# Performance work log

Hardware: AMD Instinct MI355X
Metric: run time of the kernel (lower is better)

The kernel has to match this reference:

```python
import jax, jax.numpy as jnp
import numpy as np

H, C = 4, 32            # heads, hidden_channel
HC = H * C              # 128
IN = 128                # in_channel
N = 50000               # nodes in sampled subgraph
E = 200000              # edges
USER, ITEM = 50000, 50000
UB = 200                # ubias_num == ibias_num
DIST = 501
BATCH = 1024
NEG = 0.2               # leaky_relu negative slope


def setup_inputs() -> dict:
    key = jax.random.key(0)
    keys = iter(jax.random.split(key, 64))

    def nrm(shape):
        return jax.random.normal(next(keys), shape, dtype=jnp.float32) * 0.05

    def ri(shape, hi):
        return jax.random.randint(next(keys), shape, 0, hi, dtype=jnp.int32)

    inp = {
        # int (graph) inputs
        "node_idx": ri((N,), USER + ITEM + 1),
        "edge_index": ri((2, E), N),
        "edge_type": ri((E,), 6),
        "t_offset_0": ri((E,), UB + 2),
        "t_offset_1": ri((E,), UB + 2),
        "dists_0": ri((E,), DIST),
        "dists_1": ri((E,), DIST),
        "center_nid": ri((BATCH,), N),
        # parameters
        "id_emb": nrm((USER + ITEM + 1, IN)),
        "ucenter_att_bias": nrm((UB + 2, HC)),
        "icenter_att_bias": nrm((UB + 2, HC)),
        "trans_att_bias": nrm((UB + 2, HC)),
        "ucenter_emb_bias": nrm((UB + 2, HC)),
        "icenter_emb_bias": nrm((UB + 2, HC)),
        "trans_emb_bias": nrm((UB + 2, HC)),
        "ucenter_att_bias_2": nrm((UB * 4 + 2, HC)),
        "icenter_att_bias_2": nrm((UB * 4 + 2, HC)),
        "trans_att_bias_2": nrm((UB * 4 + 2, HC)),
        "ucenter_emb_bias_2": nrm((UB * 4 + 2, HC)),
        "icenter_emb_bias_2": nrm((UB * 4 + 2, HC)),
        "trans_emb_bias_2": nrm((UB * 4 + 2, HC)),
        "udist_att_bias": nrm((DIST, HC)),
        "idist_att_bias": nrm((DIST, HC)),
        "udist_emb_bias": nrm((DIST, HC)),
        "idist_emb_bias": nrm((DIST, HC)),
        "udist_att_bias_2": nrm((DIST, HC)),
        "idist_att_bias_2": nrm((DIST, HC)),
        "udist_emb_bias_2": nrm((DIST, HC)),
        "idist_emb_bias_2": nrm((DIST, HC)),
        "trans_head": nrm((IN, HC)),
        "rnn_w": nrm((2 * HC, HC)),           # rnn_update Linear (no bias)
        "w1": nrm((HC * 2 + IN, HC)),          # pred_head layer 1
        "b1": jnp.zeros((HC,), jnp.float32),
        "w2": nrm((HC, ITEM)),                 # pred_head layer 2
        "b2": jnp.zeros((ITEM,), jnp.float32),
        # per-layer conv params (src/dst projections + attention vectors)
        "wl0": nrm((IN, HC)), "wr0": nrm((IN, HC)),
        "asrc0": nrm((H, C)), "adst0": nrm((H, C)),
        "wl1": nrm((HC, HC)), "wr1": nrm((HC, HC)),
        "asrc1": nrm((H, C)), "adst1": nrm((H, C)),
    }
    return inp


def reference(node_idx, edge_index, edge_type, t_offset_0, t_offset_1, dists_0,
              dists_1, center_nid, id_emb, ucenter_att_bias, icenter_att_bias,
              trans_att_bias, ucenter_emb_bias, icenter_emb_bias, trans_emb_bias,
              ucenter_att_bias_2, icenter_att_bias_2, trans_att_bias_2,
              ucenter_emb_bias_2, icenter_emb_bias_2, trans_emb_bias_2,
              udist_att_bias, idist_att_bias, udist_emb_bias, idist_emb_bias,
              udist_att_bias_2, idist_att_bias_2, udist_emb_bias_2,
              idist_emb_bias_2, trans_head, rnn_w, w1, b1, w2, b2,
              wl0, wr0, asrc0, adst0, wl1, wr1, asrc1, adst1):
    x = id_emb[node_idx]                       # [N, IN] gather
    src, dst = edge_index[0], edge_index[1]
    is_u = (edge_type == 0)[:, None]           # user-center homo edges
    is_homo = (edge_type < 2)[:, None]
    involved = ((edge_type == 0) | (edge_type == 2) | (edge_type == 3))[:, None]

    def edge_bias(u_tab, i_tab, tr_tab, toff):
        # homo edges: type-0 -> user table, type-1 -> item table; hetero -> trans table
        b = jnp.where(is_u, u_tab[toff], jnp.where(is_homo, i_tab[toff], tr_tab[toff]))
        return b.reshape(-1, H, C)

    def dist_bias(u_tab, i_tab, dists):
        b = jnp.where(is_u, u_tab[dists], i_tab[dists]) * involved
        return b.reshape(-1, H, C)

    att_b = [edge_bias(ucenter_att_bias, icenter_att_bias, trans_att_bias, t_offset_0),
             edge_bias(ucenter_att_bias_2, icenter_att_bias_2, trans_att_bias_2, t_offset_1)]
    emb_b = [edge_bias(ucenter_emb_bias, icenter_emb_bias, trans_emb_bias, t_offset_0),
             edge_bias(ucenter_emb_bias_2, icenter_emb_bias_2, trans_emb_bias_2, t_offset_1)]
    att_d = [dist_bias(udist_att_bias, idist_att_bias, dists_0),
             dist_bias(udist_att_bias_2, idist_att_bias_2, dists_1)]
    emb_d = [dist_bias(udist_emb_bias, idist_emb_bias, dists_0),
             dist_bias(udist_emb_bias_2, idist_emb_bias_2, dists_1)]

    n_nodes = x.shape[0]

    def conv(h, wl, wr, asrc, adst, ab, eb, ad, ed):
        k = (h @ wl).reshape(n_nodes, H, C)
        q = (h @ wr).reshape(n_nodes, H, C)
        msg = k[src] + eb + ed                                   # [E,H,C]
        logit = jax.nn.leaky_relu(
            jnp.einsum('ehc,hc->eh', k[src] + ab + ad, asrc)
            + jnp.einsum('ehc,hc->eh', q[dst], adst), NEG)        # [E,H]
        m = jax.ops.segment_max(logit, dst, num_segments=n_nodes)
        a = jnp.exp(logit - m[dst])
        den = jax.ops.segment_sum(a, dst, num_segments=n_nodes)
        alpha = a / jnp.maximum(den[dst], 1e-16)
        out = jax.ops.segment_sum(alpha[..., None] * msg, dst, num_segments=n_nodes)
        return out.reshape(n_nodes, HC)

    layers = [(wl0, wr0, asrc0, adst0), (wl1, wr1, asrc1, adst1)]
    x_inter = [x]
    cur = x
    for i in range(2):
        last = cur @ trans_head if i == 0 else cur
        wl, wr, asrc, adst = layers[i]
        cur = conv(cur, wl, wr, asrc, adst, att_b[i], emb_b[i], att_d[i], emb_d[i])
        cur = jnp.tanh(jnp.concatenate([cur, last], axis=-1) @ rnn_w)
        x_inter.append(cur)
        if i != 1:
            cur = jax.nn.relu(cur)   # dropout: eval mode -> identity

    feat = jnp.concatenate(x_inter, axis=-1)[center_nid]   # [B, 2*HC+IN]
    hdd = jax.nn.leaky_relu(feat @ w1 + b1, NEG)            # dropout eval -> identity
    logits = hdd @ w2 + b2                                  # [B, ITEM]
    return logits
```

## Files before the change

kernel.cpp:

```cpp
#include <hip/hip_runtime.h>
#include <cstdint>
#include <cstddef>

typedef unsigned short u16;
typedef __attribute__((ext_vector_type(8))) short short8;
typedef __attribute__((ext_vector_type(4))) float f32x4;

#define HC_ 128
#define CAP 32
#define OFF_U0   0
#define OFF_I0   202
#define OFF_T0   404
#define OFF_UD0  606
#define OFF_ID0  1107
#define OFF_U2   1608
#define OFF_I2   2410
#define OFF_T2   3212
#define OFF_UD2  4014
#define OFF_ID2  4515
#define DOT_ROWS 5016

__device__ __forceinline__ float b2f(u16 u) {
  union { unsigned int i; float f; } v; v.i = ((unsigned int)u) << 16; return v.f;
}
__device__ __forceinline__ u16 f2b(float f) {
  union { float f; unsigned int i; } v; v.f = f;
  unsigned int r = v.i + 0x7fffu + ((v.i >> 16) & 1u);
  return (u16)(r >> 16);
}

__global__ __launch_bounds__(256) void prolog_k(
    const int* __restrict__ nidx, const float* __restrict__ emb, u16* __restrict__ x,
    const float* u0, const float* i0, const float* t0, const float* ud0, const float* id0,
    const float* u2, const float* i2, const float* t2, const float* ud2, const float* id2,
    const float* __restrict__ asrc0, const float* __restrict__ asrc1,
    float* __restrict__ dots,
    const float* __restrict__ wr0, const float* __restrict__ adst0,
    const float* __restrict__ wr1, const float* __restrict__ adst1,
    float* __restrict__ wq,
    const float* __restrict__ rnn_w, u16* __restrict__ rnn_wb,
    const float* __restrict__ th, u16* __restrict__ Wt,
    int* __restrict__ cur, float* __restrict__ kdot0, float* __restrict__ kdot1,
    int* __restrict__ mask1, int* __restrict__ mask2,
    const int* __restrict__ center, int B_, int Nn)
{
  int b = blockIdx.x, t = threadIdx.x;
  const int nbZ    = (Nn + 16 + 255) >> 8;
  const int nbC    = (B_ + 255) >> 8;
  const int nbGx   = ((Nn + 16) * 16 + 255) >> 8;
  const int nbDots = (DOT_ROWS * 4 + 255) >> 8;

  if (b < nbZ) {
    int i = b * 256 + t;
    if (i < Nn + 16) {
      cur[i] = 0;
      f32x4 z = {0.f, 0.f, 0.f, 0.f};
      *(f32x4*)(kdot0 + (size_t)i * 4) = z;
      *(f32x4*)(kdot1 + (size_t)i * 4) = z;
    }
    return;
  }
  b -= nbZ;
  if (b < nbC) {
    int i = b * 256 + t;
    if (i < B_) { int c = center[i]; mask2[c] = 1; mask1[c] = 1; }
    return;
  }
  b -= nbC;
  if (b < nbGx) {
    int i = b * 256 + t;
    int n = i >> 4, c = (i & 15) << 3;
    if (n < Nn) {
      int id = nidx[n];
      const float* s = emb + (size_t)id * HC_ + c;
      u16 tmp[8];
#pragma unroll
      for (int j = 0; j < 8; ++j) tmp[j] = f2b(s[j]);
      *(short8*)(x + (size_t)n * HC_ + c) = *(short8*)tmp;
    } else if (n < Nn + 16) {
      short8 z = {0,0,0,0,0,0,0,0};
      *(short8*)(x + (size_t)n * HC_ + c) = z;
    }
    return;
  }
  b -= nbGx;
  if (b < nbDots) {
    int i = b * 256 + t;
    if (i < DOT_ROWS * 4) {
      int r = i >> 2, h = i & 3;
      const float* tab; int lr; const float* as;
      if      (r < OFF_I0)  { tab = u0;  lr = r;            as = asrc0; }
      else if (r < OFF_T0)  { tab = i0;  lr = r - OFF_I0;   as = asrc0; }
      else if (r < OFF_UD0) { tab = t0;  lr = r - OFF_T0;   as = asrc0; }
      else if (r < OFF_ID0) { tab = ud0; lr = r - OFF_UD0;  as = asrc0; }
      else if (r < OFF_U2)  { tab = id0; lr = r - OFF_ID0;  as = asrc0; }
      else if (r < OFF_I2)  { tab = u2;  lr = r - OFF_U2;   as = asrc1; }
      else if (r < OFF_T2)  { tab = i2;  lr = r - OFF_I2;   as = asrc1; }
      else if (r < OFF_UD2) { tab = t2;  lr = r - OFF_T2;   as = asrc1; }
      else if (r < OFF_ID2) { tab = ud2; lr = r - OFF_UD2;  as = asrc1; }
      else                  { tab = id2; lr = r - OFF_ID2;  as = asrc1; }
      float s = 0.f;
#pragma unroll
      for (int c = 0; c < 32; ++c)
        s += tab[(size_t)lr * HC_ + h * 32 + c] * as[h * 32 + c];
      dots[i] = s;
    }
    return;
  }
  b -= nbDots;
  if (b < 4) {
    int i = b * 256 + t;
    int layer = i >> 9, k = (i >> 2) & 127, h = i & 3;
    const float* wr = layer ? wr1 : wr0;
    const float* ad = layer ? adst1 : adst0;
    float s = 0.f;
#pragma unroll
    for (int c = 0; c < 32; ++c)
      s += wr[(size_t)k * HC_ + h * 32 + c] * ad[h * 32 + c];
    wq[i] = s;
    return;
  }
  b -= 4;
  if (b < 128) {
    int i = b * 256 + t;
    rnn_wb[i] = f2b(rnn_w[i]);
    return;
  }
  b -= 128;
  {
    int i = b * 256 + t;
    if (i < 16384) {
      int r = i >> 7, c = i & 127;
      float s = 0.f;
#pragma unroll 8
      for (int k = 0; k < 128; ++k)
        s += th[r * 128 + k] * rnn_w[(size_t)(128 + k) * 128 + c];
      Wt[i] = f2b(s);
    }
  }
}

__global__ void fill_k(const int* __restrict__ src, const int* __restrict__ dst,
                       const int* __restrict__ ety,
                       const int* __restrict__ toff0, const int* __restrict__ toff1,
                       const int* __restrict__ dist0, const int* __restrict__ dist1,
                       const float* __restrict__ dots,
                       int* __restrict__ cur,
                       int2* __restrict__ m0a, f32x4* __restrict__ e0a,
                       int2* __restrict__ m1a, f32x4* __restrict__ e1a,
                       const int* __restrict__ mask2, int* __restrict__ mask1, int E)
{
  int e = blockIdx.x * blockDim.x + threadIdx.x;
  if (e >= E) return;
  int d = dst[e];
  int s = src[e];
  if (mask2[d]) mask1[s] = 1;
  int slot = atomicAdd(&cur[d], 1);
  if (slot >= CAP) return;
  int ty = ety[e];
  int to0 = toff0[e], to1 = toff1[e], di0 = dist0[e], di1 = dist1[e];
  bool inv = (ty == 0 || ty == 2 || ty == 3);
  int ar0 = (ty == 0) ? (OFF_U0 + to0) : (ty < 2) ? (OFF_I0 + to0) : (OFF_T0 + to0);
  int ar1 = (ty == 0) ? (OFF_U2 + to1) : (ty < 2) ? (OFF_I2 + to1) : (OFF_T2 + to1);
  f32x4 e0 = *(const f32x4*)(dots + (size_t)ar0 * 4);
  f32x4 e1 = *(const f32x4*)(dots + (size_t)ar1 * 4);
  if (inv) {
    int dr0 = ((ty == 0) ? OFF_UD0 : OFF_ID0) + di0;
    int dr1 = ((ty == 0) ? OFF_UD2 : OFF_ID2) + di1;
    e0 += *(const f32x4*)(dots + (size_t)dr0 * 4);
    e1 += *(const f32x4*)(dots + (size_t)dr1 * 4);
  }
  size_t ix = (size_t)d * CAP + slot;
  m0a[ix] = make_int2(s, ty | (to0 << 3) | (di0 << 13));
  m1a[ix] = make_int2(s, ty | (to1 << 3) | (di1 << 13));
  e0a[ix] = e0;
  e1a[ix] = e1;
}

__global__ void mark0_k(const int* __restrict__ esrc, const int* __restrict__ edst,
                        const int* __restrict__ mask1, int* __restrict__ mask0, int E)
{
  int e = blockIdx.x * blockDim.x + threadIdx.x;
  if (e < E && mask1[edst[e]]) mask0[esrc[e]] = 1;
}

__global__ void compact_k(const int* __restrict__ mask0, const int* __restrict__ mask1,
                          int* __restrict__ L0, int* __restrict__ L1,
                          int* __restrict__ cnts, int Nn)
{
  int n = blockIdx.x * blockDim.x + threadIdx.x;
  if (n >= Nn) return;
  int m1 = mask1[n];
  if (m1 | mask0[n]) L0[atomicAdd(&cnts[0], 1)] = n;
  if (m1)            L1[atomicAdd(&cnts[1], 1)] = n;
}

template<int RELUA>
__global__ __launch_bounds__(256) void gemm_kq_g(
    const u16* __restrict__ A, const float* __restrict__ W, u16* __restrict__ C,
    const float* __restrict__ asrc, const float* __restrict__ wqt,
    float* __restrict__ kdot, float* __restrict__ qdot,
    const int* __restrict__ list, const int* __restrict__ cnts, int ci, int Nsent)
{
  const int lane = threadIdx.x & 63;
  const int wave = threadIdx.x >> 6;
  const int quad = lane >> 4;
  const int l16  = lane & 15;
  const int by   = blockIdx.y;
  const int n0   = by * 64 + wave * 16;

  short8 bfrag[4];
#pragma unroll
  for (int ks = 0; ks < 4; ++ks) {
    short8 bf;
    const int kb = ks * 32 + quad * 8;
#pragma unroll
    for (int j = 0; j < 8; ++j)
      bf[j] = (short)f2b(W[(size_t)(kb + j) * HC_ + n0 + l16]);
    bfrag[ks] = bf;
  }
  const int hh = n0 >> 5;
  const float asv = asrc[n0 + l16];

  const int cnt = cnts[ci];
  const int mtiles = (cnt + 15) >> 4;
  for (int mt = blockIdx.x; mt < mtiles; mt += gridDim.x) {
    const int rA = mt * 16 + l16;
    const int gA = (rA < cnt) ? list[rA] : Nsent;
    const u16* arow = A + (size_t)gA * HC_;
    f32x4 acc = {0.f, 0.f, 0.f, 0.f};
    float qp[4] = {0.f, 0.f, 0.f, 0.f};
#pragma unroll
    for (int ks = 0; ks < 4; ++ks) {
      short8 af = *(const short8*)(arow + ks * 32 + quad * 8);
      if (RELUA) {
#pragma unroll
        for (int j = 0; j < 8; ++j) af[j] = (af[j] < (short)0) ? (short)0 : af[j];
      }
#pragma unroll
      for (int j = 0; j < 8; ++j) {
        float v = b2f((u16)af[j]);
        const float* wr = wqt + (size_t)(ks * 32 + quad * 8 + j) * 4;
        qp[0] += v * wr[0]; qp[1] += v * wr[1];
        qp[2] += v * wr[2]; qp[3] += v * wr[3];
      }
      acc = __builtin_amdgcn_mfma_f32_16x16x32_bf16(af, bfrag[ks], acc, 0, 0, 0);
    }
#pragma unroll
    for (int h = 0; h < 4; ++h) {
      qp[h] += __shfl_xor(qp[h], 16, 64);
      qp[h] += __shfl_xor(qp[h], 32, 64);
    }
    if (by == 0 && quad == 0) {
      f32x4 qv; qv[0] = qp[0]; qv[1] = qp[1]; qv[2] = qp[2]; qv[3] = qp[3];
      *(f32x4*)(qdot + (size_t)gA * 4) = qv;
    }
    int gC[4];
#pragma unroll
    for (int r = 0; r < 4; ++r) {
      const int rC = mt * 16 + quad * 4 + r;
      gC[r] = (rC < cnt) ? list[rC] : Nsent;
    }
#pragma unroll
    for (int r = 0; r < 4; ++r) {
      float sr = acc[r] * asv;
      sr += __shfl_xor(sr, 1, 64); sr += __shfl_xor(sr, 2, 64);
      sr += __shfl_xor(sr, 4, 64); sr += __shfl_xor(sr, 8, 64);
      if (l16 == 0)
        atomicAdd(&kdot[(size_t)gC[r] * 4 + hh], sr);
    }
#pragma unroll
    for (int r = 0; r < 4; ++r)
      C[(size_t)gC[r] * HC_ + n0 + l16] = f2b(acc[r]);
  }
}

__global__ __launch_bounds__(256) void gemm2_g(
    const float* __restrict__ A1, const u16* __restrict__ W1,
    const u16* __restrict__ A2, const u16* __restrict__ W2,
    u16* __restrict__ Cout,
    const int* __restrict__ list, const int* __restrict__ cnts, int ci, int Nsent)
{
  const int lane = threadIdx.x & 63;
  const int wave = threadIdx.x >> 6;
  const int quad = lane >> 4;
  const int l16  = lane & 15;
  const int n0   = blockIdx.y * 64 + wave * 16;

  short8 bf1[4], bf2[4];
#pragma unroll
  for (int ks = 0; ks < 4; ++ks) {
    short8 a, b;
    const int kb = ks * 32 + quad * 8;
#pragma unroll
    for (int j = 0; j < 8; ++j) {
      a[j] = (short)W1[(size_t)(kb + j) * HC_ + n0 + l16];
      b[j] = (short)W2[(size_t)(kb + j) * HC_ + n0 + l16];
    }
    bf1[ks] = a; bf2[ks] = b;
  }

  const int cnt = cnts[ci];
  const int mtiles = (cnt + 15) >> 4;
  for (int mt = blockIdx.x; mt < mtiles; mt += gridDim.x) {
    const int rA = mt * 16 + l16;
    const int gA = (rA < cnt) ? list[rA] : Nsent;
    const float* a1 = A1 + (size_t)gA * HC_;
    const u16*   a2 = A2 + (size_t)gA * HC_;
    f32x4 acc = {0.f, 0.f, 0.f, 0.f};
#pragma unroll
    for (int ks = 0; ks < 4; ++ks) {
      short8 af;
      const float* p = a1 + ks * 32 + quad * 8;
#pragma unroll
      for (int j = 0; j < 8; ++j) af[j] = (short)f2b(p[j]);
      acc = __builtin_amdgcn_mfma_f32_16x16x32_bf16(af, bf1[ks], acc, 0, 0, 0);
    }
#pragma unroll
    for (int ks = 0; ks < 4; ++ks) {
      short8 af = *(const short8*)(a2 + ks * 32 + quad * 8);
      acc = __builtin_amdgcn_mfma_f32_16x16x32_bf16(af, bf2[ks], acc, 0, 0, 0);
    }
#pragma unroll
    for (int r = 0; r < 4; ++r) {
      const int rC = mt * 16 + quad * 4 + r;
      const int gC = (rC < cnt) ? list[rC] : Nsent;
      Cout[(size_t)gC * HC_ + n0 + l16] = f2b(tanhf(acc[r]));
    }
  }
}

template<int DEVCNT>
__global__ __launch_bounds__(256) void conv_k(
    const int* __restrict__ cur, const int2* __restrict__ meta,
    const f32x4* __restrict__ edot,
    const u16* __restrict__ kbuf,
    const float* __restrict__ kdot, const float* __restrict__ qdot,
    const float* __restrict__ uemb, const float* __restrict__ iemb,
    const float* __restrict__ temb,
    const float* __restrict__ udemb, const float* __restrict__ idemb,
    const int* __restrict__ list, const int* __restrict__ cnts, int ci, int cntConst,
    float* __restrict__ CO)
{
  __shared__ float als[4][CAP][4];
  const int wv = threadIdx.x >> 6;
  const int lane = threadIdx.x & 63;
  const int bound = DEVCNT ? cnts[ci] : cntConst;
  const int wstep = gridDim.x * 4;
  const int h0 = lane >> 5;
  const int h1 = h0 + 2;

  for (int wid = (blockIdx.x * blockDim.x + threadIdx.x) >> 6; wid < bound; wid += wstep) {
    const int n = list[wid];
    int cnt = cur[n]; if (cnt > CAP) cnt = CAP;
    const float q0 = qdot[n * 4 + h0];
    const float q1 = qdot[n * 4 + h1];
    const int2* mb = meta + (size_t)n * CAP;
    const f32x4* eb = edot + (size_t)n * CAP;

    float den0 = 0.f, den1 = 0.f;
    for (int e = 0; e < cnt; ++e) {
      int s = mb[e].x;
      f32x4 ed = eb[e];
      float l0 = kdot[s * 4 + h0] + q0 + ed[h0];
      float l1 = kdot[s * 4 + h1] + q1 + ed[h1];
      l0 = (l0 > 0.f) ? l0 : 0.2f * l0;
      l1 = (l1 > 0.f) ? l1 : 0.2f * l1;
      float a0 = __expf(fminf(l0, 30.f));
      float a1 = __expf(fminf(l1, 30.f));
      den0 += a0; den1 += a1;
      if ((lane & 31) == 0) { als[wv][e][h0] = a0; als[wv][e][h1] = a1; }
    }
    const float r0 = 1.f / fmaxf(den0, 1e-16f);
    const float r1 = 1.f / fmaxf(den1, 1e-16f);

    float acc0 = 0.f, acc1 = 0.f;
    for (int e = 0; e < cnt; ++e) {
      int2 mrec = mb[e];
      int s = mrec.x;
      int ty = mrec.y & 7, to = (mrec.y >> 3) & 1023, di = mrec.y >> 13;
      float al0 = als[wv][e][h0] * r0;
      float al1 = als[wv][e][h1] * r1;

      float m0 = b2f(kbuf[(size_t)s * HC_ + lane]);
      float m1 = b2f(kbuf[(size_t)s * HC_ + 64 + lane]);
      const float* et = (ty == 0) ? uemb : (ty < 2) ? iemb : temb;
      m0 += et[(size_t)to * HC_ + lane];
      m1 += et[(size_t)to * HC_ + 64 + lane];
      if (ty == 0 || ty == 2 || ty == 3) {
        const float* dt = (ty == 0) ? udemb : idemb;
        m0 += dt[(size_t)di * HC_ + lane];
        m1 += dt[(size_t)di * HC_ + 64 + lane];
      }
      acc0 += al0 * m0;
      acc1 += al1 * m1;
    }
    CO[(size_t)n * HC_ + lane]      = acc0;
    CO[(size_t)n * HC_ + 64 + lane] = acc1;
  }
}

__global__ __launch_bounds__(256) void gh_k(
    const float* __restrict__ CO, const u16* __restrict__ rnn_wb,
    const u16* __restrict__ h1, const u16* __restrict__ xb,
    const int* __restrict__ center, const float* __restrict__ w1,
    const float* __restrict__ b1, u16* __restrict__ hdd)
{
  __shared__ u16 h2s[16][136];
  const int t = threadIdx.x;
  const int lane = t & 63, wave = t >> 6, quad = lane >> 4, l16 = lane & 15;
  const int mt = blockIdx.x;
  const int rowm = mt * 16 + l16;
  const int nid = center[rowm];
  const u16* W1 = rnn_wb;
  const u16* W2 = rnn_wb + HC_ * HC_;

#pragma unroll
  for (int half = 0; half < 2; ++half) {
    const int n0 = half * 64 + wave * 16;
    short8 bf1[4], bf2[4];
#pragma unroll
    for (int ks = 0; ks < 4; ++ks) {
      short8 a, b;
      const int kb = ks * 32 + quad * 8;
#pragma unroll
      for (int j = 0; j < 8; ++j) {
        a[j] = (short)W1[(size_t)(kb + j) * HC_ + n0 + l16];
        b[j] = (short)W2[(size_t)(kb + j) * HC_ + n0 + l16];
      }
      bf1[ks] = a; bf2[ks] = b;
    }
    const float* a1 = CO + (size_t)nid * HC_;
    const u16*   a2 = h1 + (size_t)nid * HC_;
    f32x4 acc = {0.f, 0.f, 0.f, 0.f};
#pragma unroll
    for (int ks = 0; ks < 4; ++ks) {
      short8 af;
      const float* p = a1 + ks * 32 + quad * 8;
#pragma unroll
      for (int j = 0; j < 8; ++j) af[j] = (short)f2b(p[j]);
      acc = __builtin_amdgcn_mfma_f32_16x16x32_bf16(af, bf1[ks], acc, 0, 0, 0);
    }
#pragma unroll
    for (int ks = 0; ks < 4; ++ks) {
      short8 af = *(const short8*)(a2 + ks * 32 + quad * 8);
#pragma unroll
      for (int j = 0; j < 8; ++j) af[j] = (af[j] < (short)0) ? (short)0 : af[j];
      acc = __builtin_amdgcn_mfma_f32_16x16x32_bf16(af, bf2[ks], acc, 0, 0, 0);
    }
#pragma unroll
    for (int r = 0; r < 4; ++r)
      h2s[quad * 4 + r][n0 + l16] = f2b(tanhf(acc[r]));
  }
  __syncthreads();

#pragma unroll
  for (int half = 0; half < 2; ++half) {
    const int n0 = half * 64 + wave * 16;
    short8 bfrag[12];
#pragma unroll
    for (int ks = 0; ks < 12; ++ks) {
      short8 bf;
      const int kb = ks * 32 + quad * 8;
#pragma unroll
      for (int j = 0; j < 8; ++j)
        bf[j] = (short)f2b(w1[(size_t)(kb + j) * HC_ + n0 + l16]);
      bfrag[ks] = bf;
    }
    const float bv = b1[n0 + l16];
    f32x4 acc = {0.f, 0.f, 0.f, 0.f};
#pragma unroll
    for (int ks = 0; ks < 12; ++ks) {
      short8 af;
      if (ks < 4)
        af = *(const short8*)(xb + (size_t)nid * HC_ + ks * 32 + quad * 8);
      else if (ks < 8)
        af = *(const short8*)(h1 + (size_t)nid * HC_ + (ks - 4) * 32 + quad * 8);
      else
        af = *(const short8*)(&h2s[l16][(ks - 8) * 32 + quad * 8]);
      acc = __builtin_amdgcn_mfma_f32_16x16x32_bf16(af, bfrag[ks], acc, 0, 0, 0);
    }
#pragma unroll
    for (int r = 0; r < 4; ++r) {
      float v = acc[r] + bv;
      v = (v > 0.f) ? v : 0.2f * v;
      hdd[(size_t)(mt * 16 + quad * 4 + r) * HC_ + n0 + l16] = f2b(v);
    }
  }
}

__global__ __launch_bounds__(256) void gemm_out_k(
    const u16* __restrict__ A, const float* __restrict__ W,
    const float* __restrict__ bias, float* __restrict__ out, int M, int ITEM)
{
  __shared__ float lds[4][16][68];
  const int lane = threadIdx.x & 63;
  const int wv   = threadIdx.x >> 6;
  const int quad = lane >> 4;
  const int l16  = lane & 15;
  const int nbase = blockIdx.y * 256 + wv * 64;

  short8 bfrag[4][4];
#pragma unroll
  for (int nt = 0; nt < 4; ++nt) {
    const int colc = nbase + nt * 16 + l16;
    const int col = (colc < ITEM) ? colc : (ITEM - 1);
#pragma unroll
    for (int ks = 0; ks < 4; ++ks) {
      short8 bf;
      const int kb = ks * 32 + quad * 8;
#pragma unroll
      for (int j = 0; j < 8; ++j)
        bf[j] = (short)f2b(W[(size_t)(kb + j) * ITEM + col]);
      bfrag[nt][ks] = bf;
    }
  }
  const int c4 = nbase + l16 * 4;
  const bool wvalid = (c4 + 3) < ITEM;
  float4 bv = make_float4(0.f, 0.f, 0.f, 0.f);
  if (wvalid) bv = *(const float4*)(bias + c4);

  const int mtiles = M >> 4;
  for (int mt = blockIdx.x; mt < mtiles; mt += gridDim.x) {
    const u16* arow = A + (size_t)(mt * 16 + l16) * HC_;
    short8 af[4];
#pragma unroll
    for (int ks = 0; ks < 4; ++ks)
      af[ks] = *(const short8*)(arow + ks * 32 + quad * 8);
    f32x4 acc[4];
#pragma unroll
    for (int nt = 0; nt < 4; ++nt) acc[nt] = (f32x4){0.f, 0.f, 0.f, 0.f};
#pragma unroll
    for (int nt = 0; nt < 4; ++nt)
#pragma unroll
      for (int ks = 0; ks < 4; ++ks)
        acc[nt] = __builtin_amdgcn_mfma_f32_16x16x32_bf16(af[ks], bfrag[nt][ks],
                                                          acc[nt], 0, 0, 0);
#pragma unroll
    for (int nt = 0; nt < 4; ++nt)
#pragma unroll
      for (int r = 0; r < 4; ++r)
        lds[wv][quad * 4 + r][nt * 16 + l16] = acc[nt][r];
    __syncthreads();
    if (wvalid) {
#pragma unroll
      for (int i = 0; i < 4; ++i) {
        const int row = (lane >> 4) + i * 4;
        float4 v = *(const float4*)(&lds[wv][row][l16 * 4]);
        v.x += bv.x; v.y += bv.y; v.z += bv.z; v.w += bv.w;
        *(float4*)(out + (size_t)(mt * 16 + row) * ITEM + c4) = v;
      }
    }
    __syncthreads();
  }
}

extern "C" void kernel_launch(void* const* d_in, const int* in_sizes, int n_in,
                              void* d_out, int out_size, void* d_ws, size_t ws_size,
                              hipStream_t stream)
{
  (void)n_in; (void)out_size; (void)ws_size;
  const int* node_idx = (const int*)d_in[0];
  const int* eidx     = (const int*)d_in[1];
  const int* etype    = (const int*)d_in[2];
  const int* toff0    = (const int*)d_in[3];
  const int* toff1    = (const int*)d_in[4];
  const int* dist0    = (const int*)d_in[5];
  const int* dist1    = (const int*)d_in[6];
  const int* center   = (const int*)d_in[7];
  const float* id_emb   = (const float*)d_in[8];
  const float* u_att    = (const float*)d_in[9];
  const float* i_att    = (const float*)d_in[10];
  const float* t_att    = (const float*)d_in[11];
  const float* u_emb    = (const float*)d_in[12];
  const float* i_emb    = (const float*)d_in[13];
  const float* t_emb    = (const float*)d_in[14];
  const float* u_att2   = (const float*)d_in[15];
  const float* i_att2   = (const float*)d_in[16];
  const float* t_att2   = (const float*)d_in[17];
  const float* u_emb2   = (const float*)d_in[18];
  const float* i_emb2   = (const float*)d_in[19];
  const float* t_emb2   = (const float*)d_in[20];
  const float* ud_att   = (const float*)d_in[21];
  const float* id_att   = (const float*)d_in[22];
  const float* ud_emb   = (const float*)d_in[23];
  const float* id_embd  = (const float*)d_in[24];
  const float* ud_att2  = (const float*)d_in[25];
  const float* id_att2  = (const float*)d_in[26];
  const float* ud_emb2  = (const float*)d_in[27];
  const float* id_emb2  = (const float*)d_in[28];
  const float* trans_head = (const float*)d_in[29];
  const float* rnn_w    = (const float*)d_in[30];
  const float* w1       = (const float*)d_in[31];
  const float* b1       = (const float*)d_in[32];
  const float* w2       = (const float*)d_in[33];
  const float* b2       = (const float*)d_in[34];
  const float* wl0      = (const float*)d_in[35];
  const float* wr0      = (const float*)d_in[36];
  const float* asrc0    = (const float*)d_in[37];
  const float* adst0    = (const float*)d_in[38];
  const float* wl1      = (const float*)d_in[39];
  const float* wr1      = (const float*)d_in[40];
  const float* asrc1    = (const float*)d_in[41];
  const float* adst1    = (const float*)d_in[42];

  const int N_    = in_sizes[0];
  const int E_    = in_sizes[2];
  const int B_    = in_sizes[7];
  const int ITEM_ = in_sizes[34];
  const int* esrc = eidx;
  const int* edst = eidx + E_;

  char* ws = (char*)d_ws;
  size_t off = 0;
  auto alloc = [&](size_t bytes) -> char* {
    char* p = ws + off;
    off += (bytes + 255) & ~(size_t)255;
    return p;
  };
  const int NS = N_ + 16;
  float* CO_b  = (float*)alloc((size_t)NS * HC_ * 4);
  u16*   k_b   = (u16*)  alloc((size_t)NS * HC_ * 2);
  u16*   x_b   = (u16*)  alloc((size_t)NS * HC_ * 2);
  u16*   h1_b  = (u16*)  alloc((size_t)NS * HC_ * 2);
  float* kdot0 = (float*)alloc((size_t)NS * 4 * 4);
  float* kdot1 = (float*)alloc((size_t)NS * 4 * 4);
  float* qdot  = (float*)alloc((size_t)NS * 4 * 4);
  float* dots  = (float*)alloc((size_t)DOT_ROWS * 4 * 4);
  float* wq    = (float*)alloc(1024 * 4);
  u16*   rnn_wb= (u16*)  alloc(256 * HC_ * 2);
  u16*   Wt    = (u16*)  alloc(HC_ * HC_ * 2);
  u16*   hdd   = (u16*)  alloc((size_t)B_ * HC_ * 2);
  int*   cur   = (int*)  alloc((size_t)NS * 4);
  int2*  m0a   = (int2*) alloc((size_t)N_ * CAP * 8);
  int2*  m1a   = (int2*) alloc((size_t)N_ * CAP * 8);
  f32x4* e0a   = (f32x4*)alloc((size_t)N_ * CAP * 16);
  f32x4* e1a   = (f32x4*)alloc((size_t)N_ * CAP * 16);
  int*   maskb = (int*)  alloc(((size_t)3 * N_ + 2) * 4);
  int*   mask0 = maskb;
  int*   mask1 = maskb + N_;
  int*   mask2 = maskb + 2 * N_;
  int*   cnts  = maskb + 3 * N_;
  int*   L0    = (int*)  alloc((size_t)N_ * 4);
  int*   L1    = (int*)  alloc((size_t)N_ * 4);

  const int TB = 256;
  auto nb = [&](long long t) { return (int)((t + TB - 1) / TB); };

  hipMemsetAsync(maskb, 0, ((size_t)3 * N_ + 2) * 4, stream);

  const int nbZ    = (N_ + 16 + 255) / 256;
  const int nbC    = (B_ + 255) / 256;
  const int nbGx   = ((N_ + 16) * 16 + 255) / 256;
  const int nbDots = (DOT_ROWS * 4 + 255) / 256;
  const int prologBlocks = nbZ + nbC + nbGx + nbDots + 4 + 128 + 64;
  prolog_k<<<prologBlocks, TB, 0, stream>>>(
      node_idx, id_emb, x_b,
      u_att, i_att, t_att, ud_att, id_att,
      u_att2, i_att2, t_att2, ud_att2, id_att2,
      asrc0, asrc1, dots,
      wr0, adst0, wr1, adst1, wq,
      rnn_w, rnn_wb, trans_head, Wt,
      cur, kdot0, kdot1,
      mask1, mask2, center, B_, N_);

  fill_k<<<nb(E_), TB, 0, stream>>>(esrc, edst, etype, toff0, toff1, dist0, dist1,
                                    dots, cur, m0a, e0a, m1a, e1a, mask2, mask1, E_);

  mark0_k<<<nb(E_), TB, 0, stream>>>(esrc, edst, mask1, mask0, E_);
  compact_k<<<nb(N_), TB, 0, stream>>>(mask0, mask1, L0, L1, cnts, N_);

  gemm_kq_g<0><<<dim3(640, 2), TB, 0, stream>>>(
      x_b, wl0, k_b, asrc0, wq, kdot0, qdot, L0, cnts, 0, N_);

  conv_k<1><<<1536, TB, 0, stream>>>(
      cur, m0a, e0a, k_b, kdot0, qdot,
      u_emb, i_emb, t_emb, ud_emb, id_embd, L1, cnts, 1, 0, CO_b);

  gemm2_g<<<dim3(640, 2), TB, 0, stream>>>(CO_b, rnn_wb, x_b, Wt, h1_b,
                                           L1, cnts, 1, N_);

  gemm_kq_g<1><<<dim3(640, 2), TB, 0, stream>>>(
      h1_b, wl1, k_b, asrc1, wq + 512, kdot1, qdot, L1, cnts, 1, N_);

  conv_k<0><<<nb((long long)B_ * 64), TB, 0, stream>>>(
      cur, m1a, e1a, k_b, kdot1, qdot,
      u_emb2, i_emb2, t_emb2, ud_emb2, id_emb2, center, nullptr, 0, B_, CO_b);

  gh_k<<<B_ / 16, TB, 0, stream>>>(CO_b, rnn_wb, h1_b, x_b, center, w1, b1, hdd);

  gemm_out_k<<<dim3(8, (ITEM_ + 255) / 256), TB, 0, stream>>>(
      hdd, w2, b2, (float*)d_out, B_, ITEM_);
}
```

Baseline: 559.5 us.

## Fuse final-layer attention conv into head kernel, drop syncs, retune grids

```diff
diff --git a/kernel.cpp b/kernel.cpp
--- a/kernel.cpp
+++ b/kernel.cpp
@@ -330,7 +330,6 @@
   }
 }
 
-template<int DEVCNT>
 __global__ __launch_bounds__(256) void conv_k(
     const int* __restrict__ cur, const int2* __restrict__ meta,
     const f32x4* __restrict__ edot,
@@ -339,13 +338,13 @@
     const float* __restrict__ uemb, const float* __restrict__ iemb,
     const float* __restrict__ temb,
     const float* __restrict__ udemb, const float* __restrict__ idemb,
-    const int* __restrict__ list, const int* __restrict__ cnts, int ci, int cntConst,
+    const int* __restrict__ list, const int* __restrict__ cnts, int ci,
     float* __restrict__ CO)
 {
   __shared__ float als[4][CAP][4];
   const int wv = threadIdx.x >> 6;
   const int lane = threadIdx.x & 63;
-  const int bound = DEVCNT ? cnts[ci] : cntConst;
+  const int bound = cnts[ci];
   const int wstep = gridDim.x * 4;
   const int h0 = lane >> 5;
   const int h1 = h0 + 2;
@@ -400,24 +399,85 @@
   }
 }
 
-__global__ __launch_bounds__(256) void gh_k(
-    const float* __restrict__ CO, const u16* __restrict__ rnn_wb,
-    const u16* __restrict__ h1, const u16* __restrict__ xb,
-    const int* __restrict__ center, const float* __restrict__ w1,
-    const float* __restrict__ b1, u16* __restrict__ hdd)
-{
+__global__ __launch_bounds__(256) void ghc_k(
+    const int* __restrict__ cur, const int2* __restrict__ meta,
+    const f32x4* __restrict__ edot,
+    const u16* __restrict__ kbuf,
+    const float* __restrict__ kdot, const float* __restrict__ qdot,
+    const float* __restrict__ uemb, const float* __restrict__ iemb,
+    const float* __restrict__ temb,
+    const float* __restrict__ udemb, const float* __restrict__ idemb,
+    const int* __restrict__ center,
+    const u16* __restrict__ rnn_wb, const u16* __restrict__ h1b,
+    const u16* __restrict__ xb,
+    const float* __restrict__ w1, const float* __restrict__ b1,
+    u16* __restrict__ hdd)
+{
+  __shared__ float co_s[16][132];
   __shared__ u16 h2s[16][136];
+  __shared__ float als[4][CAP][4];
   const int t = threadIdx.x;
-  const int lane = t & 63, wave = t >> 6, quad = lane >> 4, l16 = lane & 15;
+  const int lane = t & 63, wv = t >> 6, quad = lane >> 4, l16 = lane & 15;
   const int mt = blockIdx.x;
+  const int h0 = lane >> 5, h1h = h0 + 2;
+
+  for (int r = wv; r < 16; r += 4) {
+    const int n = center[mt * 16 + r];
+    int cnt = cur[n]; if (cnt > CAP) cnt = CAP;
+    const float q0 = qdot[n * 4 + h0];
+    const float q1 = qdot[n * 4 + h1h];
+    const int2* mb = meta + (size_t)n * CAP;
+    const f32x4* eb = edot + (size_t)n * CAP;
+
+    float den0 = 0.f, den1 = 0.f;
+    for (int e = 0; e < cnt; ++e) {
+      int s = mb[e].x;
+      f32x4 ed = eb[e];
+      float l0 = kdot[s * 4 + h0] + q0 + ed[h0];
+      float l1 = kdot[s * 4 + h1h] + q1 + ed[h1h];
+      l0 = (l0 > 0.f) ? l0 : 0.2f * l0;
+      l1 = (l1 > 0.f) ? l1 : 0.2f * l1;
+      float a0 = __expf(fminf(l0, 30.f));
+      float a1 = __expf(fminf(l1, 30.f));
+      den0 += a0; den1 += a1;
+      if ((lane & 31) == 0) { als[wv][e][h0] = a0; als[wv][e][h1h] = a1; }
+    }
+    const float r0 = 1.f / fmaxf(den0, 1e-16f);
+    const float r1 = 1.f / fmaxf(den1, 1e-16f);
+
+    float acc0 = 0.f, acc1 = 0.f;
+    for (int e = 0; e < cnt; ++e) {
+      int2 mrec = mb[e];
+      int s = mrec.x;
+      int ty = mrec.y & 7, to = (mrec.y >> 3) & 1023, di = mrec.y >> 13;
+      float al0 = als[wv][e][h0] * r0;
+      float al1 = als[wv][e][h1h] * r1;
+
+      float m0 = b2f(kbuf[(size_t)s * HC_ + lane]);
+      float m1 = b2f(kbuf[(size_t)s * HC_ + 64 + lane]);
+      const float* et = (ty == 0) ? uemb : (ty < 2) ? iemb : temb;
+      m0 += et[(size_t)to * HC_ + lane];
+      m1 += et[(size_t)to * HC_ + 64 + lane];
+      if (ty == 0 || ty == 2 || ty == 3) {
+        const float* dt = (ty == 0) ? udemb : idemb;
+        m0 += dt[(size_t)di * HC_ + lane];
+        m1 += dt[(size_t)di * HC_ + 64 + lane];
+      }
+      acc0 += al0 * m0;
+      acc1 += al1 * m1;
+    }
+    co_s[r][lane]      = acc0;
+    co_s[r][64 + lane] = acc1;
+  }
+  __syncthreads();
+
   const int rowm = mt * 16 + l16;
   const int nid = center[rowm];
   const u16* W1 = rnn_wb;
   const u16* W2 = rnn_wb + HC_ * HC_;
-
 #pragma unroll
   for (int half = 0; half < 2; ++half) {
-    const int n0 = half * 64 + wave * 16;
+    const int n0 = half * 64 + wv * 16;
     short8 bf1[4], bf2[4];
 #pragma unroll
     for (int ks = 0; ks < 4; ++ks) {
@@ -430,15 +490,13 @@
       }
       bf1[ks] = a; bf2[ks] = b;
     }
-    const float* a1 = CO + (size_t)nid * HC_;
-    const u16*   a2 = h1 + (size_t)nid * HC_;
+    const u16* a2 = h1b + (size_t)nid * HC_;
     f32x4 acc = {0.f, 0.f, 0.f, 0.f};
 #pragma unroll
     for (int ks = 0; ks < 4; ++ks) {
       short8 af;
-      const float* p = a1 + ks * 32 + quad * 8;
-#pragma unroll
-      for (int j = 0; j < 8; ++j) af[j] = (short)f2b(p[j]);
+#pragma unroll
+      for (int j = 0; j < 8; ++j) af[j] = (short)f2b(co_s[l16][ks * 32 + quad * 8 + j]);
       acc = __builtin_amdgcn_mfma_f32_16x16x32_bf16(af, bf1[ks], acc, 0, 0, 0);
     }
 #pragma unroll
@@ -456,7 +514,7 @@
 
 #pragma unroll
   for (int half = 0; half < 2; ++half) {
-    const int n0 = half * 64 + wave * 16;
+    const int n0 = half * 64 + wv * 16;
     short8 bfrag[12];
 #pragma unroll
     for (int ks = 0; ks < 12; ++ks) {
@@ -475,7 +533,7 @@
       if (ks < 4)
         af = *(const short8*)(xb + (size_t)nid * HC_ + ks * 32 + quad * 8);
       else if (ks < 8)
-        af = *(const short8*)(h1 + (size_t)nid * HC_ + (ks - 4) * 32 + quad * 8);
+        af = *(const short8*)(h1b + (size_t)nid * HC_ + (ks - 4) * 32 + quad * 8);
       else
         af = *(const short8*)(&h2s[l16][(ks - 8) * 32 + quad * 8]);
       acc = __builtin_amdgcn_mfma_f32_16x16x32_bf16(af, bfrag[ks], acc, 0, 0, 0);
@@ -541,7 +599,6 @@
 #pragma unroll
       for (int r = 0; r < 4; ++r)
         lds[wv][quad * 4 + r][nt * 16 + l16] = acc[nt][r];
-    __syncthreads();
     if (wvalid) {
 #pragma unroll
       for (int i = 0; i < 4; ++i) {
@@ -551,7 +608,6 @@
         *(float4*)(out + (size_t)(mt * 16 + row) * ITEM + c4) = v;
       }
     }
-    __syncthreads();
   }
 }
 
@@ -673,22 +729,21 @@
   gemm_kq_g<0><<<dim3(640, 2), TB, 0, stream>>>(
       x_b, wl0, k_b, asrc0, wq, kdot0, qdot, L0, cnts, 0, N_);
 
-  conv_k<1><<<1536, TB, 0, stream>>>(
+  conv_k<<<1536, TB, 0, stream>>>(
       cur, m0a, e0a, k_b, kdot0, qdot,
-      u_emb, i_emb, t_emb, ud_emb, id_embd, L1, cnts, 1, 0, CO_b);
-
-  gemm2_g<<<dim3(640, 2), TB, 0, stream>>>(CO_b, rnn_wb, x_b, Wt, h1_b,
+      u_emb, i_emb, t_emb, ud_emb, id_embd, L1, cnts, 1, CO_b);
+
+  gemm2_g<<<dim3(192, 2), TB, 0, stream>>>(CO_b, rnn_wb, x_b, Wt, h1_b,
                                            L1, cnts, 1, N_);
 
-  gemm_kq_g<1><<<dim3(640, 2), TB, 0, stream>>>(
+  gemm_kq_g<1><<<dim3(192, 2), TB, 0, stream>>>(
       h1_b, wl1, k_b, asrc1, wq + 512, kdot1, qdot, L1, cnts, 1, N_);
 
-  conv_k<0><<<nb((long long)B_ * 64), TB, 0, stream>>>(
+  ghc_k<<<B_ / 16, TB, 0, stream>>>(
       cur, m1a, e1a, k_b, kdot1, qdot,
-      u_emb2, i_emb2, t_emb2, ud_emb2, id_emb2, center, nullptr, 0, B_, CO_b);
-
-  gh_k<<<B_ / 16, TB, 0, stream>>>(CO_b, rnn_wb, h1_b, x_b, center, w1, b1, hdd);
-
-  gemm_out_k<<<dim3(8, (ITEM_ + 255) / 256), TB, 0, stream>>>(
+      u_emb2, i_emb2, t_emb2, ud_emb2, id_emb2, center,
+      rnn_wb, h1_b, x_b, w1, b1, hdd);
+
+  gemm_out_k<<<dim3(4, (ITEM_ + 255) / 256), TB, 0, stream>>>(
       hdd, w2, b2, (float*)d_out, B_, ITEM_);
 }
```

Result: no change. 562.5 us (+0.5%).
